# Kernel tuning notes

Measured on AMD Instinct MI355X. Metric: run time of the kernel, lower is better.

The kernel has to match this reference:

```python
import jax, jax.numpy as jnp
import numpy as np

N_NODES = 100000
N_EDGES = 1600000
D = 128
NEG_SLOPE = 0.2


def setup_inputs() -> dict:
    key = jax.random.key(0)
    k1, k2, k3, k4, k5, k6 = jax.random.split(key, 6)
    x = jax.random.normal(k1, (N_NODES, D), dtype=jnp.float32)
    src = jax.random.randint(k2, (N_EDGES,), 0, N_NODES)
    dst = jax.random.randint(k3, (N_EDGES,), 0, N_NODES)
    # torch.nn.Linear default init: U(-1/sqrt(fan_in), 1/sqrt(fan_in))
    W = jax.random.uniform(k4, (D, D), dtype=jnp.float32, minval=-1.0, maxval=1.0) / np.sqrt(D)
    a_left = jax.random.uniform(k5, (1, D), dtype=jnp.float32, minval=-1.0, maxval=1.0) / np.sqrt(D)
    a_right = jax.random.uniform(k6, (1, D), dtype=jnp.float32, minval=-1.0, maxval=1.0) / np.sqrt(D)
    return {"x": x, "src": src, "dst": dst, "W": W, "a_left": a_left, "a_right": a_right}


def reference(x, src, dst, W, a_left, a_right):
    n = x.shape[0]
    # node-wise projections
    h = x @ W.T                      # [N, D]
    e_l = h @ a_left.T               # [N, 1]
    e_r = h @ a_right.T              # [N, 1]
    # edge attention logits: u_add_v then leaky_relu
    e = e_l[src] + e_r[dst]          # [E, 1]
    e = jnp.where(e >= 0, e, NEG_SLOPE * e)
    # edge softmax over incoming edges of each destination node
    e = e[:, 0]
    m = jax.ops.segment_max(e, dst, num_segments=n)          # [N]
    m = jnp.where(jnp.isfinite(m), m, 0.0)                   # guard empty segments
    ex = jnp.exp(e - m[dst])                                 # [E]
    denom = jax.ops.segment_sum(ex, dst, num_segments=n)     # [N]
    alpha = ex / jnp.maximum(denom[dst], 1e-38)              # [E]
    # weighted aggregation: sum_e h[src] * alpha -> dst
    msg = h[src] * alpha[:, None]                            # [E, D]
    out = jax.ops.segment_sum(msg, dst, num_segments=n)      # [N, D]
    return out
```

## Files before the change

### kernel.cpp

```cpp
#include <hip/hip_runtime.h>
#include <math.h>

#define N_NODES 100000
#define N_EDGES 1600000
#define D 128
#define NEG_SLOPE_F 0.2f
#define BK 32
#define NB3 3125
#define NHW 1563
#define ECAP 1024
#define BEPB 8192
#define BITERS (BEPB / 1024)
#define NBINB 196
#define NGEMM 1563
#define DYN_LDS 18816

typedef short short8 __attribute__((ext_vector_type(8)));
typedef float f32x4 __attribute__((ext_vector_type(4)));

__device__ __forceinline__ unsigned short f2bf_rtn(float f) {
    unsigned int u = __float_as_uint(f);
    u += 0x7fffu + ((u >> 16) & 1u);
    return (unsigned short)(u >> 16);
}
__device__ __forceinline__ float bf2f(unsigned short h) {
    return __uint_as_float((unsigned)h << 16);
}

__global__ __launch_bounds__(256) void fused_prep(
        const int* __restrict__ src, const int* __restrict__ dst,
        const float* __restrict__ x, const float* __restrict__ W,
        const float* __restrict__ a_l, const float* __restrict__ a_r,
        unsigned* __restrict__ gcount, unsigned* __restrict__ binned,
        unsigned short* __restrict__ hb, float* __restrict__ e_l,
        float* __restrict__ e_r) {
    extern __shared__ __align__(16) char smem[];
    int tid = threadIdx.x;

    if (blockIdx.x < NBINB) {
        unsigned* histp  = (unsigned*)smem;
        unsigned* startb = (unsigned*)(smem + 6256);
        for (int i = tid; i < NHW; i += 256) histp[i] = 0;
        __syncthreads();
        int base = blockIdx.x * BEPB;
        const int4* d4 = (const int4*)dst;
        const int4* s4 = (const int4*)src;
        int i40 = base >> 2;
        for (int it = 0; it < BITERS; ++it) {
            int i4 = i40 + it * 256 + tid;
            if (i4 * 4 < N_EDGES) {
                int4 v = d4[i4];
#define CNT(dd) { int b = (dd) >> 5; atomicAdd(&histp[b >> 1], (b & 1) ? 65536u : 1u); }
                CNT(v.x) CNT(v.y) CNT(v.z) CNT(v.w)
#undef CNT
            }
        }
        __syncthreads();
        for (int b = tid; b < NB3; b += 256) {
            unsigned c = (histp[b >> 1] >> ((b & 1) * 16)) & 0xffffu;
            startb[b] = c ? atomicAdd(&gcount[b], c) : 0u;
        }
        __syncthreads();
        for (int i = tid; i < NHW; i += 256) histp[i] = 0;
        __syncthreads();
        for (int it = 0; it < BITERS; ++it) {
            int i4 = i40 + it * 256 + tid;
            if (i4 * 4 < N_EDGES) {
                int4 dv = d4[i4];
                int4 sv = s4[i4];
#define PUT(dd, ss)                                                          \
                {                                                            \
                    int b = (dd) >> 5;                                       \
                    unsigned old = atomicAdd(&histp[b >> 1],                 \
                                             (b & 1) ? 65536u : 1u);         \
                    unsigned r = startb[b] +                                 \
                                 ((old >> ((b & 1) * 16)) & 0xffffu);        \
                    if (r < ECAP)                                            \
                        binned[(size_t)b * ECAP + r] =                       \
                            ((unsigned)((dd) & 31) << 17) | (unsigned)(ss);  \
                }
                PUT(dv.x, sv.x) PUT(dv.y, sv.y) PUT(dv.z, sv.z) PUT(dv.w, sv.w)
#undef PUT
            }
        }
        return;
    }

    unsigned short (*Bh)[136] = (unsigned short(*)[136])smem;
    unsigned short (*Bl)[136] = (unsigned short(*)[136])(smem + 8704);
    int lane = tid & 63, wid = tid >> 6;
    int p = lane & 15, g = lane >> 4;
    int row0 = (blockIdx.x - NBINB) * 64;
    int n = N_NODES;

    int arow = row0 + wid * 16 + p;
    int arow_c = min(arow, n - 1);
    const float4* X4 = (const float4*)x;
    float4 xa0[4], xa1[4];
#pragma unroll
    for (int kc = 0; kc < 4; ++kc) {
        size_t bi = (size_t)arow_c * 32 + kc * 8 + g * 2;
        xa0[kc] = X4[bi];
        xa1[kc] = X4[bi + 1];
    }
    short8 ah[4];
#pragma unroll
    for (int kc = 0; kc < 4; ++kc) {
        short8 a;
        a[0] = (short)f2bf_rtn(xa0[kc].x);
        a[1] = (short)f2bf_rtn(xa0[kc].y);
        a[2] = (short)f2bf_rtn(xa0[kc].z);
        a[3] = (short)f2bf_rtn(xa0[kc].w);
        a[4] = (short)f2bf_rtn(xa1[kc].x);
        a[5] = (short)f2bf_rtn(xa1[kc].y);
        a[6] = (short)f2bf_rtn(xa1[kc].z);
        a[7] = (short)f2bf_rtn(xa1[kc].w);
        ah[kc] = a;
    }

    f32x4 acc[4][2];
#pragma unroll
    for (int qt = 0; qt < 4; ++qt)
#pragma unroll
        for (int ct = 0; ct < 2; ++ct) acc[qt][ct] = (f32x4)(0.f);

    const float4* W4 = (const float4*)W;

#pragma unroll
    for (int qt = 0; qt < 4; ++qt) {
        __syncthreads();
        for (int q2 = 0; q2 < 4; ++q2) {
            int idx = q2 * 256 + tid;
            int r = idx >> 5, c4 = idx & 31;
            float4 v = W4[((size_t)(qt * 32 + r)) * 32 + c4];
            ushort4 hh, ll;
            hh.x = f2bf_rtn(v.x); ll.x = f2bf_rtn(v.x - bf2f(hh.x));
            hh.y = f2bf_rtn(v.y); ll.y = f2bf_rtn(v.y - bf2f(hh.y));
            hh.z = f2bf_rtn(v.z); ll.z = f2bf_rtn(v.z - bf2f(hh.z));
            hh.w = f2bf_rtn(v.w); ll.w = f2bf_rtn(v.w - bf2f(hh.w));
            *(ushort4*)&Bh[r][c4 * 4] = hh;
            *(ushort4*)&Bl[r][c4 * 4] = ll;
        }
        __syncthreads();

#pragma unroll
        for (int kc = 0; kc < 4; ++kc) {
            int cb = kc * 32 + g * 8;
#pragma unroll
            for (int ct = 0; ct < 2; ++ct) {
                short8 bh = *(const short8*)&Bh[ct * 16 + p][cb];
                short8 bl = *(const short8*)&Bl[ct * 16 + p][cb];
                acc[qt][ct] = __builtin_amdgcn_mfma_f32_16x16x32_bf16(ah[kc], bh, acc[qt][ct], 0, 0, 0);
                acc[qt][ct] = __builtin_amdgcn_mfma_f32_16x16x32_bf16(ah[kc], bl, acc[qt][ct], 0, 0, 0);
            }
        }
    }

    float al8[4][2], ar8[4][2];
#pragma unroll
    for (int qt = 0; qt < 4; ++qt)
#pragma unroll
        for (int ct = 0; ct < 2; ++ct) {
            al8[qt][ct] = a_l[qt * 32 + ct * 16 + p];
            ar8[qt][ct] = a_r[qt * 32 + ct * 16 + p];
        }
#pragma unroll
    for (int i = 0; i < 4; ++i) {
        int gr = row0 + wid * 16 + g * 4 + i;
        bool ok = gr < n;
        float pl = 0.f, pr = 0.f;
        if (ok) {
#pragma unroll
            for (int qt = 0; qt < 4; ++qt)
#pragma unroll
                for (int ct = 0; ct < 2; ++ct) {
                    float v = acc[qt][ct][i];
                    hb[(size_t)gr * 128 + qt * 32 + ct * 16 + p] = f2bf_rtn(v);
                    pl += v * al8[qt][ct];
                    pr += v * ar8[qt][ct];
                }
        }
#pragma unroll
        for (int o = 8; o; o >>= 1) {
            pl += __shfl_xor(pl, o);
            pr += __shfl_xor(pr, o);
        }
        if (ok && p == 0) { e_l[gr] = pl; e_r[gr] = pr; }
    }
}

__global__ __launch_bounds__(256) void bucket_fused(
        const unsigned short* __restrict__ hb, const float* __restrict__ e_l,
        const float* __restrict__ e_r, const unsigned* __restrict__ gcount,
        const unsigned* __restrict__ binned, float* __restrict__ out) {
    __shared__ unsigned es[ECAP];
    __shared__ float    ee[ECAP];
    __shared__ unsigned short sidx[ECAP];
    __shared__ unsigned cntl[BK];
    __shared__ unsigned startl[BK];
    __shared__ unsigned curl[BK];
    __shared__ float    erl[BK];
    __shared__ int   lds_s[4][64];
    __shared__ float lds_e[4][64];

    int tid = threadIdx.x, lane = tid & 63, w = tid >> 6;
    int g = lane >> 4, p = lane & 15;
    int b = blockIdx.x, d0 = b * BK;
    size_t rs = (size_t)b * ECAP;
    int cnt = min((int)gcount[b], ECAP);

    if (tid < BK) {
        int d = d0 + tid;
        erl[tid] = (d < N_NODES) ? e_r[d] : 0.f;
        cntl[tid] = 0u;
    }
    __syncthreads();

#define ACC8(hv, xe)                                                        \
    acc[0] += xe * __uint_as_float(hv.x << 16);                             \
    acc[1] += xe * __uint_as_float(hv.x & 0xffff0000u);                     \
    acc[2] += xe * __uint_as_float(hv.y << 16);                             \
    acc[3] += xe * __uint_as_float(hv.y & 0xffff0000u);                     \
    acc[4] += xe * __uint_as_float(hv.z << 16);                             \
    acc[5] += xe * __uint_as_float(hv.z & 0xffff0000u);                     \
    acc[6] += xe * __uint_as_float(hv.w << 16);                             \
    acc[7] += xe * __uint_as_float(hv.w & 0xffff0000u);

    for (int i = tid; i < cnt; i += 256) {
        unsigned v = binned[rs + i];
        unsigned ld = v >> 17;
        float e = e_l[v & 0x1ffffu] + erl[ld];
        e = (e >= 0.f) ? e : NEG_SLOPE_F * e;
        es[i] = v;
        ee[i] = __expf(e);
        atomicAdd(&cntl[ld], 1u);
    }
    __syncthreads();
    if (tid < BK) {
        unsigned c = cntl[tid];
        unsigned inc = c;
#pragma unroll
        for (int o = 1; o < BK; o <<= 1) {
            unsigned nv = __shfl_up(inc, o);
            if (lane >= o) inc += nv;
        }
        startl[tid] = inc - c;
        curl[tid] = inc - c;
    }
    __syncthreads();
    for (int i = tid; i < cnt; i += 256) {
        unsigned ld = es[i] >> 17;
        unsigned pos = atomicAdd(&curl[ld], 1u);
        sidx[pos] = (unsigned short)i;
    }
    __syncthreads();
    for (int k = 0; k < BK / 4; ++k) {
        int ld = (k << 2) | w;
        int start = (int)startl[ld];
        int deg = (int)cntl[ld];

        float denom = 0.f;
        float acc[8];
#pragma unroll
        for (int q = 0; q < 8; ++q) acc[q] = 0.f;
        for (int b2 = 0; b2 < deg; b2 += 64) {
            int kk = b2 + lane;
            bool valid = kk < deg;
            int i = valid ? sidx[start + kk] : 0;
            float ex = valid ? ee[i] : 0.f;
            denom += ex;
            lds_s[w][lane] = valid ? (int)(es[i] & 0x1ffffu) : 0;
            lds_e[w][lane] = ex;
            asm volatile("s_waitcnt lgkmcnt(0)" ::: "memory");
            int c2 = min(64, deg - b2);
            int nst = (c2 + 3) >> 2;
            int u = 0;
            for (; u + 4 <= nst; u += 4) {
                int j0 = u * 4 + g;
                int s0 = lds_s[w][j0];       float x0 = lds_e[w][j0];
                int s1 = lds_s[w][j0 + 4];   float x1 = lds_e[w][j0 + 4];
                int s2 = lds_s[w][j0 + 8];   float x2 = lds_e[w][j0 + 8];
                int s3 = lds_s[w][j0 + 12];  float x3 = lds_e[w][j0 + 12];
                uint4 h0 = *(const uint4*)&hb[(size_t)s0 * 128 + p * 8];
                uint4 h1 = *(const uint4*)&hb[(size_t)s1 * 128 + p * 8];
                uint4 h2 = *(const uint4*)&hb[(size_t)s2 * 128 + p * 8];
                uint4 h3 = *(const uint4*)&hb[(size_t)s3 * 128 + p * 8];
                ACC8(h0, x0) ACC8(h1, x1) ACC8(h2, x2) ACC8(h3, x3)
            }
            for (; u < nst; ++u) {
                int j = u * 4 + g;
                int sj = lds_s[w][j];
                float xj = lds_e[w][j];
                uint4 hv = *(const uint4*)&hb[(size_t)sj * 128 + p * 8];
                ACC8(hv, xj)
            }
        }
#pragma unroll
        for (int q = 0; q < 8; ++q) {
            acc[q] += __shfl_xor(acc[q], 16);
            acc[q] += __shfl_xor(acc[q], 32);
        }
#pragma unroll
        for (int o = 32; o; o >>= 1) denom += __shfl_xor(denom, o);
        float inv = 1.f / fmaxf(denom, 1e-38f);
        int d = d0 + ld;
        if (g == 0 && d < N_NODES) {
            f32x4 o0 = {acc[0] * inv, acc[1] * inv, acc[2] * inv, acc[3] * inv};
            f32x4 o1 = {acc[4] * inv, acc[5] * inv, acc[6] * inv, acc[7] * inv};
            __builtin_nontemporal_store(o0, (f32x4*)&out[(size_t)d * 128 + p * 8]);
            __builtin_nontemporal_store(o1, (f32x4*)&out[(size_t)d * 128 + p * 8 + 4]);
        }
    }
#undef ACC8
}

extern "C" void kernel_launch(void* const* d_in, const int* in_sizes, int n_in,
                              void* d_out, int out_size, void* d_ws, size_t ws_size,
                              hipStream_t stream) {
    const float* x   = (const float*)d_in[0];
    const int*   src = (const int*)d_in[1];
    const int*   dst = (const int*)d_in[2];
    const float* W   = (const float*)d_in[3];
    const float* a_l = (const float*)d_in[4];
    const float* a_r = (const float*)d_in[5];
    float* out = (float*)d_out;

    char* ws = (char*)d_ws;
    unsigned short* hb = (unsigned short*)ws; ws += (size_t)N_NODES * D * 2;
    float*    e_l    = (float*)ws;    ws += (size_t)N_NODES * 4;
    float*    e_r    = (float*)ws;    ws += (size_t)N_NODES * 4;
    unsigned* gcount = (unsigned*)ws; ws += (size_t)NB3 * 4;
    unsigned* binned = (unsigned*)ws; ws += (size_t)NB3 * ECAP * 4;

    hipMemsetAsync(gcount, 0, (size_t)NB3 * 4, stream);

    fused_prep<<<NBINB + NGEMM, 256, DYN_LDS, stream>>>(
        src, dst, x, W, a_l, a_r, gcount, binned, hb, e_l, e_r);
    bucket_fused<<<NB3, 256, 0, stream>>>(hb, e_l, e_r, gcount, binned, out);
}
```

Measured before the change: 112.2 us.

## Scatter edges directly into sorted LDS order, drop index indirection and staging

The bucket kernel now keeps each thread's edges in registers during the count phase. It then scatters the packed edge word and its exp value straight into per-destination sorted LDS arrays, instead of writing unsorted arrays plus a sorted index array. The aggregation loop reads edge source ids and weights directly from the sorted arrays with clamped indices, which removes the per-wave staging buffers and the double LDS indirection. The denominator is computed in a separate pass. Register-held edges assume at most 4 per thread (ECAP 1024 / 256), and the change adds a little extra LDS traffic for the denominator pass.

```diff
diff --git a/kernel.cpp b/kernel.cpp
--- a/kernel.cpp
+++ b/kernel.cpp
@@ -193,15 +193,12 @@
         const unsigned short* __restrict__ hb, const float* __restrict__ e_l,
         const float* __restrict__ e_r, const unsigned* __restrict__ gcount,
         const unsigned* __restrict__ binned, float* __restrict__ out) {
-    __shared__ unsigned es[ECAP];
-    __shared__ float    ee[ECAP];
-    __shared__ unsigned short sidx[ECAP];
+    __shared__ unsigned es2[ECAP + 4];
+    __shared__ float    ee2[ECAP + 4];
     __shared__ unsigned cntl[BK];
     __shared__ unsigned startl[BK];
     __shared__ unsigned curl[BK];
     __shared__ float    erl[BK];
-    __shared__ int   lds_s[4][64];
-    __shared__ float lds_e[4][64];
 
     int tid = threadIdx.x, lane = tid & 63, w = tid >> 6;
     int g = lane >> 4, p = lane & 15;
@@ -213,6 +210,44 @@
         int d = d0 + tid;
         erl[tid] = (d < N_NODES) ? e_r[d] : 0.f;
         cntl[tid] = 0u;
+    }
+    __syncthreads();
+
+    unsigned vreg[4];
+    float xreg[4];
+    int nheld = 0;
+#pragma unroll
+    for (int k = 0; k < 4; ++k) {
+        int i = tid + k * 256;
+        if (i < cnt) {
+            unsigned v = __builtin_nontemporal_load(&binned[rs + i]);
+            unsigned ld = v >> 17;
+            float e = e_l[v & 0x1ffffu] + erl[ld];
+            e = (e >= 0.f) ? e : NEG_SLOPE_F * e;
+            vreg[nheld] = v;
+            xreg[nheld] = __expf(e);
+            ++nheld;
+            atomicAdd(&cntl[ld], 1u);
+        }
+    }
+    __syncthreads();
+    if (tid < BK) {
+        unsigned c = cntl[tid];
+        unsigned inc = c;
+#pragma unroll
+        for (int o = 1; o < BK; o <<= 1) {
+            unsigned nv = __shfl_up(inc, o);
+            if (lane >= o) inc += nv;
+        }
+        startl[tid] = inc - c;
+        curl[tid] = inc - c;
+    }
+    __syncthreads();
+    for (int k = 0; k < nheld; ++k) {
+        unsigned v = vreg[k];
+        unsigned pos = atomicAdd(&curl[v >> 17], 1u);
+        es2[pos] = v;
+        ee2[pos] = xreg[k];
     }
     __syncthreads();
 
@@ -226,82 +261,52 @@
     acc[6] += xe * __uint_as_float(hv.w << 16);                             \
     acc[7] += xe * __uint_as_float(hv.w & 0xffff0000u);
 
-    for (int i = tid; i < cnt; i += 256) {
-        unsigned v = binned[rs + i];
-        unsigned ld = v >> 17;
-        float e = e_l[v & 0x1ffffu] + erl[ld];
-        e = (e >= 0.f) ? e : NEG_SLOPE_F * e;
-        es[i] = v;
-        ee[i] = __expf(e);
-        atomicAdd(&cntl[ld], 1u);
-    }
-    __syncthreads();
-    if (tid < BK) {
-        unsigned c = cntl[tid];
-        unsigned inc = c;
-#pragma unroll
-        for (int o = 1; o < BK; o <<= 1) {
-            unsigned nv = __shfl_up(inc, o);
-            if (lane >= o) inc += nv;
-        }
-        startl[tid] = inc - c;
-        curl[tid] = inc - c;
-    }
-    __syncthreads();
-    for (int i = tid; i < cnt; i += 256) {
-        unsigned ld = es[i] >> 17;
-        unsigned pos = atomicAdd(&curl[ld], 1u);
-        sidx[pos] = (unsigned short)i;
-    }
-    __syncthreads();
     for (int k = 0; k < BK / 4; ++k) {
         int ld = (k << 2) | w;
         int start = (int)startl[ld];
         int deg = (int)cntl[ld];
 
         float denom = 0.f;
+        for (int kk = lane; kk < deg; kk += 64) denom += ee2[start + kk];
+#pragma unroll
+        for (int o = 32; o; o >>= 1) denom += __shfl_xor(denom, o);
+
         float acc[8];
 #pragma unroll
         for (int q = 0; q < 8; ++q) acc[q] = 0.f;
-        for (int b2 = 0; b2 < deg; b2 += 64) {
-            int kk = b2 + lane;
-            bool valid = kk < deg;
-            int i = valid ? sidx[start + kk] : 0;
-            float ex = valid ? ee[i] : 0.f;
-            denom += ex;
-            lds_s[w][lane] = valid ? (int)(es[i] & 0x1ffffu) : 0;
-            lds_e[w][lane] = ex;
-            asm volatile("s_waitcnt lgkmcnt(0)" ::: "memory");
-            int c2 = min(64, deg - b2);
-            int nst = (c2 + 3) >> 2;
-            int u = 0;
-            for (; u + 4 <= nst; u += 4) {
-                int j0 = u * 4 + g;
-                int s0 = lds_s[w][j0];       float x0 = lds_e[w][j0];
-                int s1 = lds_s[w][j0 + 4];   float x1 = lds_e[w][j0 + 4];
-                int s2 = lds_s[w][j0 + 8];   float x2 = lds_e[w][j0 + 8];
-                int s3 = lds_s[w][j0 + 12];  float x3 = lds_e[w][j0 + 12];
-                uint4 h0 = *(const uint4*)&hb[(size_t)s0 * 128 + p * 8];
-                uint4 h1 = *(const uint4*)&hb[(size_t)s1 * 128 + p * 8];
-                uint4 h2 = *(const uint4*)&hb[(size_t)s2 * 128 + p * 8];
-                uint4 h3 = *(const uint4*)&hb[(size_t)s3 * 128 + p * 8];
-                ACC8(h0, x0) ACC8(h1, x1) ACC8(h2, x2) ACC8(h3, x3)
-            }
-            for (; u < nst; ++u) {
-                int j = u * 4 + g;
-                int sj = lds_s[w][j];
-                float xj = lds_e[w][j];
-                uint4 hv = *(const uint4*)&hb[(size_t)sj * 128 + p * 8];
-                ACC8(hv, xj)
-            }
-        }
+
+        int nst = (deg + 3) >> 2;
+        int u = 0;
+        for (; u + 4 <= nst; u += 4) {
+            int j0 = u * 4 + g;
+            int j1 = j0 + 4, j2 = j0 + 8, j3 = j0 + 12;
+            int jc0 = min(j0, deg - 1), jc1 = min(j1, deg - 1);
+            int jc2 = min(j2, deg - 1), jc3 = min(j3, deg - 1);
+            unsigned v0 = es2[start + jc0]; float x0 = (j0 < deg) ? ee2[start + jc0] : 0.f;
+            unsigned v1 = es2[start + jc1]; float x1 = (j1 < deg) ? ee2[start + jc1] : 0.f;
+            unsigned v2 = es2[start + jc2]; float x2 = (j2 < deg) ? ee2[start + jc2] : 0.f;
+            unsigned v3 = es2[start + jc3]; float x3 = (j3 < deg) ? ee2[start + jc3] : 0.f;
+            uint4 h0 = *(const uint4*)&hb[(size_t)(v0 & 0x1ffffu) * 128 + p * 8];
+            uint4 h1 = *(const uint4*)&hb[(size_t)(v1 & 0x1ffffu) * 128 + p * 8];
+            uint4 h2 = *(const uint4*)&hb[(size_t)(v2 & 0x1ffffu) * 128 + p * 8];
+            uint4 h3 = *(const uint4*)&hb[(size_t)(v3 & 0x1ffffu) * 128 + p * 8];
+            ACC8(h0, x0) ACC8(h1, x1) ACC8(h2, x2) ACC8(h3, x3)
+        }
+        for (; u < nst; ++u) {
+            int j = u * 4 + g;
+            int jc = min(j, deg - 1);
+            unsigned v = es2[start + jc];
+            float xj = (j < deg) ? ee2[start + jc] : 0.f;
+            uint4 hv = *(const uint4*)&hb[(size_t)(v & 0x1ffffu) * 128 + p * 8];
+            ACC8(hv, xj)
+        }
+#undef ACC8
+
 #pragma unroll
         for (int q = 0; q < 8; ++q) {
             acc[q] += __shfl_xor(acc[q], 16);
             acc[q] += __shfl_xor(acc[q], 32);
         }
-#pragma unroll
-        for (int o = 32; o; o >>= 1) denom += __shfl_xor(denom, o);
         float inv = 1.f / fmaxf(denom, 1e-38f);
         int d = d0 + ld;
         if (g == 0 && d < N_NODES) {
@@ -311,7 +316,6 @@
             __builtin_nontemporal_store(o1, (f32x4*)&out[(size_t)d * 128 + p * 8 + 4]);
         }
     }
-#undef ACC8
 }
 
 extern "C" void kernel_launch(void* const* d_in, const int* in_sizes, int n_in,
```

Result: slower. 114.4 us (median of 2 runs) (+2.0%).
